# Kernel optimization log

Measured on AMD Instinct MI355X. Metric: run time of the kernel, lower is better.

The kernel has to match this reference:

```python
import jax, jax.numpy as jnp
import numpy as np

N_NODES = 20000
N_EDGES = 150000


def _nnconv(x, src, dst, edge_attr, nn_W, nn_b, root, bias, in_c, out_c):
    # Edge-conditioned conv (PyG NNConv, aggr='add'):
    #   W_e = edge_nn(edge_attr_e).reshape(in_c, out_c)
    #   out_i = sum_{e: dst(e)=i} x_{src(e)} @ W_e + x_i @ root + bias
    E = edge_attr.shape[0]
    W = (edge_attr @ nn_W.T + nn_b).reshape(E, in_c, out_c)  # [E, in_c, out_c]
    xj = x[src]                                              # gather [E, in_c]
    msg = jnp.einsum('ei,eio->eo', xj, W)                    # per-edge matmul
    aggr = jax.ops.segment_sum(msg, dst, num_segments=x.shape[0])
    return aggr + x @ root + bias


def setup_inputs() -> dict:
    key = jax.random.key(0)
    ks = jax.random.split(key, 20)

    def glorot(k, shape):
        fan = sum(shape)
        return jax.random.normal(k, shape, dtype=jnp.float32) * jnp.sqrt(2.0 / fan)

    x = jax.random.normal(ks[0], (N_NODES, 2), dtype=jnp.float32)
    edge_index = jax.random.randint(ks[1], (2, N_EDGES), 0, N_NODES, dtype=jnp.int64)
    edge_attr = jax.random.normal(ks[2], (N_EDGES, 2), dtype=jnp.float32)

    return {
        'x': x, 'edge_index': edge_index, 'edge_attr': edge_attr,
        # conv1: in=2, out=32, edge-net Linear(2, 64)
        'nn1_W': glorot(ks[3], (64, 2)), 'nn1_b': jnp.zeros((64,), jnp.float32),
        'root1': glorot(ks[4], (2, 32)), 'b1': jnp.zeros((32,), jnp.float32),
        # conv2: in=32, out=32, edge-net Linear(2, 1024)
        'nn2_W': glorot(ks[5], (1024, 2)), 'nn2_b': jnp.zeros((1024,), jnp.float32),
        'root2': glorot(ks[6], (32, 32)), 'b2': jnp.zeros((32,), jnp.float32),
        # conv3: in=32, out=32, edge-net Linear(2, 1024)
        'nn3_W': glorot(ks[7], (1024, 2)), 'nn3_b': jnp.zeros((1024,), jnp.float32),
        'root3': glorot(ks[8], (32, 32)), 'b3': jnp.zeros((32,), jnp.float32),
        # dense head
        'fc1_W': glorot(ks[9], (32, 32)), 'fc1_b': jnp.zeros((32,), jnp.float32),
        'fc2_W': glorot(ks[10], (1, 32)), 'fc2_b': jnp.zeros((1,), jnp.float32),
    }


def reference(x, edge_index, edge_attr,
              nn1_W, nn1_b, root1, b1,
              nn2_W, nn2_b, root2, b2,
              nn3_W, nn3_b, root3, b3,
              fc1_W, fc1_b, fc2_W, fc2_b):
    src, dst = edge_index[0], edge_index[1]
    h = jax.nn.relu(_nnconv(x, src, dst, edge_attr, nn1_W, nn1_b, root1, b1, 2, 32))
    h = jax.nn.relu(_nnconv(h, src, dst, edge_attr, nn2_W, nn2_b, root2, b2, 32, 32))
    h = jax.nn.relu(_nnconv(h, src, dst, edge_attr, nn3_W, nn3_b, root3, b3, 32, 32))
    h = jax.nn.relu(h @ fc1_W.T + fc1_b)
    return h @ fc2_W.T + fc2_b  # [N_NODES, 1]
```

## Files before the change

kernel.cpp:

```cpp
#include <hip/hip_runtime.h>


#define CAP 32

typedef float f32x4 __attribute__((ext_vector_type(4)));
typedef short s16x8 __attribute__((ext_vector_type(8)));

__device__ __forceinline__ unsigned short f2bf(float x) {
    unsigned u = __float_as_uint(x);
    unsigned r = u + 0x7FFFu + ((u >> 16) & 1u);
    return (unsigned short)(r >> 16);
}
__device__ __forceinline__ float bf2f(unsigned short h) {
    return __uint_as_float(((unsigned)h) << 16);
}

__global__ __launch_bounds__(256) void zero_kernel(int* p, int n) {
    int i = blockIdx.x * 256 + threadIdx.x;
    if (i < n) p[i] = 0;
}

__global__ __launch_bounds__(256) void scatter_kernel(
    const int* __restrict__ src, const int* __restrict__ dst,
    const float* __restrict__ ea, int* __restrict__ cnt,
    int4* __restrict__ edges, int E) {
    int tid = blockIdx.x * 256 + threadIdx.x;
    int T = gridDim.x * 256;
#pragma unroll 4
    for (int k = 0; k < 4; ++k) {
        int e = tid + k * T;
        if (e < E) {
            int d = dst[e];
            int p = atomicAdd(&cnt[d], 1);
            if (p < CAP) {
                float2 a = ((const float2*)ea)[e];
                int s = src[e];
                int4 ed;
                ed.x = s;
                ed.y = __float_as_int(a.x);
                ed.z = __float_as_int(a.y);
                ed.w = s * 32;
                edges[((size_t)d << 5) + p] = ed;
            }
        }
    }
}

__global__ __launch_bounds__(256) void conv1_kernel(
    const float* __restrict__ x, const int* __restrict__ cnt,
    const int4* __restrict__ edges, const float* __restrict__ nnW,
    const float* __restrict__ nnb, const float* __restrict__ root,
    const float* __restrict__ bias, float* __restrict__ hout, int N) {
    int tid = threadIdx.x;
    int g = tid >> 5, lane = tid & 31;
    int n = blockIdx.x * 8 + g;
    if (n >= N) return;
    int deg = cnt[n];
    deg = (deg < CAP) ? deg : CAP;
    const int4* ep = &edges[(size_t)n << 5];
    float p0 = 0, p1 = 0, q0 = 0, q1 = 0, r0 = 0, r1 = 0;
    for (int p = 0; p < deg; p += 8) {
        int m = deg - p;
        m = (m > 8) ? 8 : m;
        int4 e[8];
        float2 xv[8];
#pragma unroll
        for (int k = 0; k < 8; ++k)
            if (k < m) e[k] = ep[p + k];
#pragma unroll
        for (int k = 0; k < 8; ++k)
            if (k < m) xv[k] = ((const float2*)x)[e[k].x];
#pragma unroll
        for (int k = 0; k < 8; ++k)
            if (k < m) {
                float a0 = __int_as_float(e[k].y), a1 = __int_as_float(e[k].z);
                p0 = fmaf(a0, xv[k].x, p0);
                p1 = fmaf(a0, xv[k].y, p1);
                q0 = fmaf(a1, xv[k].x, q0);
                q1 = fmaf(a1, xv[k].y, q1);
                r0 += xv[k].x;
                r1 += xv[k].y;
            }
    }
    float acc = bias[lane];
    acc = fmaf(p0, nnW[lane * 2], acc);
    acc = fmaf(p1, nnW[(32 + lane) * 2], acc);
    acc = fmaf(q0, nnW[lane * 2 + 1], acc);
    acc = fmaf(q1, nnW[(32 + lane) * 2 + 1], acc);
    acc = fmaf(r0, nnb[lane], acc);
    acc = fmaf(r1, nnb[32 + lane], acc);
    float2 xn = ((const float2*)x)[n];
    acc = fmaf(xn.x, root[lane], acc);
    acc = fmaf(xn.y, root[32 + lane], acc);
    hout[n * 32 + lane] = fmaxf(acc, 0.f);
}

template <int BS>
__device__ __forceinline__ void stage_weights(
    const float* __restrict__ nnW, const float* __restrict__ nnb,
    const float* __restrict__ root, unsigned short (*Whi)[32][32],
    unsigned short (*Wlo)[32][32], int t) {
    for (int idx = t; idx < 4096; idx += BS) {
        int kc = idx >> 10, r = idx & 1023, k = r >> 5, o = r & 31;
        float v = (kc == 0)   ? nnW[(k * 32 + o) * 2]
                  : (kc == 1) ? nnW[(k * 32 + o) * 2 + 1]
                  : (kc == 2) ? nnb[k * 32 + o]
                              : root[k * 32 + o];
        unsigned short hb = f2bf(v);
        Whi[kc][o][k] = hb;
        Wlo[kc][o][k] = f2bf(v - bf2f(hb));
    }
}

#define MFMA_BF16 __builtin_amdgcn_mfma_f32_16x16x32_bf16

__device__ __forceinline__ void gather_to_lds(
    const float* __restrict__ h, const int* __restrict__ cnt,
    const int4* __restrict__ edges, float (*Sl)[132], int base, int t, int N) {
    int g = t >> 5, lane = t & 31;
    int n = base + g;
    float s0 = 0, s1 = 0, s2 = 0, s3 = 0;
    if (n < N) {
        int deg = cnt[n];
        deg = (deg < CAP) ? deg : CAP;
        const int4* ep = &edges[(size_t)n << 5];
        for (int p = 0; p < deg; p += 8) {
            int m = deg - p;
            m = (m > 8) ? 8 : m;
            int4 e[8];
            float hv[8];
#pragma unroll
            for (int k = 0; k < 8; ++k)
                if (k < m) e[k] = ep[p + k];
#pragma unroll
            for (int k = 0; k < 8; ++k)
                if (k < m) hv[k] = h[e[k].w + lane];
#pragma unroll
            for (int k = 0; k < 8; ++k)
                if (k < m) {
                    s0 = fmaf(__int_as_float(e[k].y), hv[k], s0);
                    s1 = fmaf(__int_as_float(e[k].z), hv[k], s1);
                    s2 += hv[k];
                }
        }
        s3 = h[n * 32 + lane];
    }
    Sl[g][lane] = s0;
    Sl[g][32 + lane] = s1;
    Sl[g][64 + lane] = s2;
    Sl[g][96 + lane] = s3;
}

__device__ __forceinline__ void tile_mfma(
    const float (*Sl)[132], const unsigned short (*Whi)[32][32],
    const unsigned short (*Wlo)[32][32], int q, int c, f32x4* acc0, f32x4* acc1) {
#pragma unroll
    for (int kc = 0; kc < 4; ++kc) {
        const float* sp = &Sl[c][kc * 32 + q * 8];
        s16x8 ah, al;
#pragma unroll
        for (int e = 0; e < 8; ++e) {
            float v = sp[e];
            unsigned short hb = f2bf(v);
            ah[e] = (short)hb;
            al[e] = (short)f2bf(v - bf2f(hb));
        }
        s16x8 bh0 = *reinterpret_cast<const s16x8*>(&Whi[kc][c][q * 8]);
        s16x8 bl0 = *reinterpret_cast<const s16x8*>(&Wlo[kc][c][q * 8]);
        s16x8 bh1 = *reinterpret_cast<const s16x8*>(&Whi[kc][16 + c][q * 8]);
        s16x8 bl1 = *reinterpret_cast<const s16x8*>(&Wlo[kc][16 + c][q * 8]);
        *acc0 = MFMA_BF16(ah, bh0, *acc0, 0, 0, 0);
        *acc0 = MFMA_BF16(al, bh0, *acc0, 0, 0, 0);
        *acc0 = MFMA_BF16(ah, bl0, *acc0, 0, 0, 0);
        *acc1 = MFMA_BF16(ah, bh1, *acc1, 0, 0, 0);
        *acc1 = MFMA_BF16(al, bh1, *acc1, 0, 0, 0);
        *acc1 = MFMA_BF16(ah, bl1, *acc1, 0, 0, 0);
    }
}

__global__ __launch_bounds__(512) void fused2_kernel(
    const float* __restrict__ h, const int* __restrict__ cnt,
    const int4* __restrict__ edges, const float* __restrict__ nnW,
    const float* __restrict__ nnb, const float* __restrict__ root,
    const float* __restrict__ bias, float* __restrict__ hout, int N) {
    __shared__ unsigned short Whi[4][32][32], Wlo[4][32][32];
    __shared__ float Sl[16][132];
    int t = threadIdx.x;
    int base = blockIdx.x * 16;
    stage_weights<512>(nnW, nnb, root, Whi, Wlo, t);
    gather_to_lds(h, cnt, edges, Sl, base, t, N);
    __syncthreads();
    if (t < 64) {
        int q = t >> 4, c = t & 15;
        f32x4 acc0 = {0.f, 0.f, 0.f, 0.f}, acc1 = {0.f, 0.f, 0.f, 0.f};
        tile_mfma(Sl, Whi, Wlo, q, c, &acc0, &acc1);
        float bb0 = bias[c], bb1 = bias[16 + c];
#pragma unroll
        for (int rr = 0; rr < 4; ++rr) {
            int n = base + q * 4 + rr;
            if (n < N) {
                hout[(size_t)n * 32 + c] = fmaxf(acc0[rr] + bb0, 0.f);
                hout[(size_t)n * 32 + 16 + c] = fmaxf(acc1[rr] + bb1, 0.f);
            }
        }
    }
}

__global__ __launch_bounds__(512) void fused3_kernel(
    const float* __restrict__ h, const int* __restrict__ cnt,
    const int4* __restrict__ edges, const float* __restrict__ nnW,
    const float* __restrict__ nnb, const float* __restrict__ root,
    const float* __restrict__ bias, const float* __restrict__ fc1W,
    const float* __restrict__ fc1b, const float* __restrict__ fc2W,
    const float* __restrict__ fc2b, float* __restrict__ out, int N) {
    __shared__ unsigned short Whi[4][32][32], Wlo[4][32][32];
    __shared__ float Sl[16][132];
    __shared__ unsigned short Th[16][32], Tl[16][32];
    int t = threadIdx.x;
    int base = blockIdx.x * 16;
    stage_weights<512>(nnW, nnb, root, Whi, Wlo, t);
    gather_to_lds(h, cnt, edges, Sl, base, t, N);
    __syncthreads();
    int q = t >> 4, c = t & 15;
    if (t < 64) {
        f32x4 acc0 = {0.f, 0.f, 0.f, 0.f}, acc1 = {0.f, 0.f, 0.f, 0.f};
        tile_mfma(Sl, Whi, Wlo, q, c, &acc0, &acc1);
        float bb0 = bias[c], bb1 = bias[16 + c];
#pragma unroll
        for (int rr = 0; rr < 4; ++rr) {
            int row = q * 4 + rr;
            float v0 = fmaxf(acc0[rr] + bb0, 0.f);
            float v1 = fmaxf(acc1[rr] + bb1, 0.f);
            unsigned short hb;
            hb = f2bf(v0); Th[row][c] = hb;      Tl[row][c] = f2bf(v0 - bf2f(hb));
            hb = f2bf(v1); Th[row][16 + c] = hb; Tl[row][16 + c] = f2bf(v1 - bf2f(hb));
        }
    }
    __syncthreads();
    if (t < 64) {
        s16x8 fh[2], fl[2];
#pragma unroll
        for (int nc = 0; nc < 2; ++nc)
#pragma unroll
            for (int e = 0; e < 8; ++e) {
                float v = fc1W[(nc * 16 + c) * 32 + q * 8 + e];
                unsigned short hb = f2bf(v);
                fh[nc][e] = (short)hb;
                fl[nc][e] = (short)f2bf(v - bf2f(hb));
            }
        s16x8 hh = *reinterpret_cast<const s16x8*>(&Th[c][q * 8]);
        s16x8 hl = *reinterpret_cast<const s16x8*>(&Tl[c][q * 8]);
        f32x4 z0 = {0.f, 0.f, 0.f, 0.f}, z1 = {0.f, 0.f, 0.f, 0.f};
        z0 = MFMA_BF16(hh, fh[0], z0, 0, 0, 0);
        z0 = MFMA_BF16(hl, fh[0], z0, 0, 0, 0);
        z0 = MFMA_BF16(hh, fl[0], z0, 0, 0, 0);
        z1 = MFMA_BF16(hh, fh[1], z1, 0, 0, 0);
        z1 = MFMA_BF16(hl, fh[1], z1, 0, 0, 0);
        z1 = MFMA_BF16(hh, fl[1], z1, 0, 0, 0);
        float f1b0 = fc1b[c], f1b1 = fc1b[16 + c];
        float w20 = fc2W[c], w21 = fc2W[16 + c];
        float f2b = fc2b[0];
#pragma unroll
        for (int rr = 0; rr < 4; ++rr) {
            float zz0 = fmaxf(z0[rr] + f1b0, 0.f);
            float zz1 = fmaxf(z1[rr] + f1b1, 0.f);
            float v = fmaf(zz0, w20, zz1 * w21);
            v += __shfl_xor(v, 1);
            v += __shfl_xor(v, 2);
            v += __shfl_xor(v, 4);
            v += __shfl_xor(v, 8);
            int n = base + q * 4 + rr;
            if (c == 0 && n < N) out[n] = v + f2b;
        }
    }
}

static inline size_t align256(size_t v) { return (v + 255) & ~(size_t)255; }

extern "C" void kernel_launch(void* const* d_in, const int* in_sizes, int n_in,
                              void* d_out, int out_size, void* d_ws, size_t ws_size,
                              hipStream_t stream) {
    const float* x = (const float*)d_in[0];
    const int* ei = (const int*)d_in[1];
    const float* ea = (const float*)d_in[2];
    const float* nn1W = (const float*)d_in[3];
    const float* nn1b = (const float*)d_in[4];
    const float* root1 = (const float*)d_in[5];
    const float* b1 = (const float*)d_in[6];
    const float* nn2W = (const float*)d_in[7];
    const float* nn2b = (const float*)d_in[8];
    const float* root2 = (const float*)d_in[9];
    const float* b2 = (const float*)d_in[10];
    const float* nn3W = (const float*)d_in[11];
    const float* nn3b = (const float*)d_in[12];
    const float* root3 = (const float*)d_in[13];
    const float* b3 = (const float*)d_in[14];
    const float* fc1W = (const float*)d_in[15];
    const float* fc1b = (const float*)d_in[16];
    const float* fc2W = (const float*)d_in[17];
    const float* fc2b = (const float*)d_in[18];

    const int N = in_sizes[0] / 2;
    const int E = in_sizes[2] / 2;
    const int* src = ei;
    const int* dst = ei + E;

    char* w = (char*)d_ws;
    int* cnt = (int*)w;     w += align256((size_t)N * 4);
    int4* edges = (int4*)w; w += align256((size_t)N * CAP * 16);
    float* h1 = (float*)w;  w += align256((size_t)N * 32 * 4);
    float* h2 = (float*)w;  w += align256((size_t)N * 32 * 4);

    float* out = (float*)d_out;

    zero_kernel<<<(N + 255) / 256, 256, 0, stream>>>(cnt, N);

    int sb = (E + 1023) / 1024;
    scatter_kernel<<<sb, 256, 0, stream>>>(src, dst, ea, cnt, edges, E);

    int gb = (N + 7) / 8;
    int fb = (N + 15) / 16;
    conv1_kernel<<<gb, 256, 0, stream>>>(x, cnt, edges, nn1W, nn1b, root1, b1, h1, N);
    fused2_kernel<<<fb, 512, 0, stream>>>(h1, cnt, edges, nn2W, nn2b, root2, b2, h2, N);
    fused3_kernel<<<fb, 512, 0, stream>>>(h2, cnt, edges, nn3W, nn3b, root3, b3,
                                          fc1W, fc1b, fc2W, fc2b, out, N);
}
```

Measured before the change: 77.31 us.

## Zero-pad edge buckets and load edge records once per lane with shuffles

The zero kernel now clears the whole edge-bucket array along with the counts, so unused slots hold zero weight and offset zero. Each aggregation loop can then run to a multiple of 8 with no per-edge bounds checks. Each lane loads one edge record, broadcasts fields with shuffles, and uses a stored 1.0 weight for the sum term. The cost is zeroing about 10 MB of buckets on every call, plus extra gathers on the padded slots.

```diff
diff --git a/kernel.cpp b/kernel.cpp
--- a/kernel.cpp
+++ b/kernel.cpp
@@ -15,9 +15,11 @@
     return __uint_as_float(((unsigned)h) << 16);
 }
 
-__global__ __launch_bounds__(256) void zero_kernel(int* p, int n) {
+__global__ __launch_bounds__(256) void zero_kernel(int4* p, int n4) {
     int i = blockIdx.x * 256 + threadIdx.x;
-    if (i < n) p[i] = 0;
+    int gt = gridDim.x * 256;
+    int4 z = {0, 0, 0, 0};
+    for (; i < n4; i += gt) p[i] = z;
 }
 
 __global__ __launch_bounds__(256) void scatter_kernel(
@@ -34,12 +36,11 @@
             int p = atomicAdd(&cnt[d], 1);
             if (p < CAP) {
                 float2 a = ((const float2*)ea)[e];
-                int s = src[e];
                 int4 ed;
-                ed.x = s;
+                ed.x = __float_as_int(1.0f);
                 ed.y = __float_as_int(a.x);
                 ed.z = __float_as_int(a.y);
-                ed.w = s * 32;
+                ed.w = src[e] * 32;
                 edges[((size_t)d << 5) + p] = ed;
             }
         }
@@ -57,30 +58,30 @@
     if (n >= N) return;
     int deg = cnt[n];
     deg = (deg < CAP) ? deg : CAP;
+    int deg8 = (deg + 7) & ~7;
     const int4* ep = &edges[(size_t)n << 5];
+    int4 rec = ep[lane];
     float p0 = 0, p1 = 0, q0 = 0, q1 = 0, r0 = 0, r1 = 0;
-    for (int p = 0; p < deg; p += 8) {
-        int m = deg - p;
-        m = (m > 8) ? 8 : m;
-        int4 e[8];
+    for (int p = 0; p < deg8; p += 8) {
         float2 xv[8];
-#pragma unroll
-        for (int k = 0; k < 8; ++k)
-            if (k < m) e[k] = ep[p + k];
-#pragma unroll
-        for (int k = 0; k < 8; ++k)
-            if (k < m) xv[k] = ((const float2*)x)[e[k].x];
-#pragma unroll
-        for (int k = 0; k < 8; ++k)
-            if (k < m) {
-                float a0 = __int_as_float(e[k].y), a1 = __int_as_float(e[k].z);
-                p0 = fmaf(a0, xv[k].x, p0);
-                p1 = fmaf(a0, xv[k].y, p1);
-                q0 = fmaf(a1, xv[k].x, q0);
-                q1 = fmaf(a1, xv[k].y, q1);
-                r0 += xv[k].x;
-                r1 += xv[k].y;
-            }
+        float a0[8], a1[8], ww[8];
+#pragma unroll
+        for (int j = 0; j < 8; ++j) {
+            int off = __shfl(rec.w, p + j, 32);
+            a0[j] = __int_as_float(__shfl(rec.y, p + j, 32));
+            a1[j] = __int_as_float(__shfl(rec.z, p + j, 32));
+            ww[j] = __int_as_float(__shfl(rec.x, p + j, 32));
+            xv[j] = ((const float2*)x)[off >> 5];
+        }
+#pragma unroll
+        for (int j = 0; j < 8; ++j) {
+            p0 = fmaf(a0[j], xv[j].x, p0);
+            p1 = fmaf(a0[j], xv[j].y, p1);
+            q0 = fmaf(a1[j], xv[j].x, q0);
+            q1 = fmaf(a1[j], xv[j].y, q1);
+            r0 = fmaf(ww[j], xv[j].x, r0);
+            r1 = fmaf(ww[j], xv[j].y, r1);
+        }
     }
     float acc = bias[lane];
     acc = fmaf(p0, nnW[lane * 2], acc);
@@ -123,27 +124,27 @@
     if (n < N) {
         int deg = cnt[n];
         deg = (deg < CAP) ? deg : CAP;
+        int deg8 = (deg + 7) & ~7;
         const int4* ep = &edges[(size_t)n << 5];
-        for (int p = 0; p < deg; p += 8) {
-            int m = deg - p;
-            m = (m > 8) ? 8 : m;
-            int4 e[8];
-            float hv[8];
-#pragma unroll
-            for (int k = 0; k < 8; ++k)
-                if (k < m) e[k] = ep[p + k];
-#pragma unroll
-            for (int k = 0; k < 8; ++k)
-                if (k < m) hv[k] = h[e[k].w + lane];
-#pragma unroll
-            for (int k = 0; k < 8; ++k)
-                if (k < m) {
-                    s0 = fmaf(__int_as_float(e[k].y), hv[k], s0);
-                    s1 = fmaf(__int_as_float(e[k].z), hv[k], s1);
-                    s2 += hv[k];
-                }
-        }
+        int4 rec = ep[lane];
         s3 = h[n * 32 + lane];
+        for (int p = 0; p < deg8; p += 8) {
+            float hv[8], a0[8], a1[8], ww[8];
+#pragma unroll
+            for (int j = 0; j < 8; ++j) {
+                int off = __shfl(rec.w, p + j, 32);
+                a0[j] = __int_as_float(__shfl(rec.y, p + j, 32));
+                a1[j] = __int_as_float(__shfl(rec.z, p + j, 32));
+                ww[j] = __int_as_float(__shfl(rec.x, p + j, 32));
+                hv[j] = h[off + lane];
+            }
+#pragma unroll
+            for (int j = 0; j < 8; ++j) {
+                s0 = fmaf(a0[j], hv[j], s0);
+                s1 = fmaf(a1[j], hv[j], s1);
+                s2 = fmaf(ww[j], hv[j], s2);
+            }
+        }
     }
     Sl[g][lane] = s0;
     Sl[g][32 + lane] = s1;
@@ -308,12 +309,14 @@
     char* w = (char*)d_ws;
     int* cnt = (int*)w;     w += align256((size_t)N * 4);
     int4* edges = (int4*)w; w += align256((size_t)N * CAP * 16);
+    char* zero_end = w;
     float* h1 = (float*)w;  w += align256((size_t)N * 32 * 4);
     float* h2 = (float*)w;  w += align256((size_t)N * 32 * 4);
 
     float* out = (float*)d_out;
 
-    zero_kernel<<<(N + 255) / 256, 256, 0, stream>>>(cnt, N);
+    int n4 = (int)((zero_end - (char*)cnt) / 16);
+    zero_kernel<<<512, 256, 0, stream>>>((int4*)cnt, n4);
 
     int sb = (E + 1023) / 1024;
     scatter_kernel<<<sb, 256, 0, stream>>>(src, dst, ea, cnt, edges, E);
```

After: 70.58 us. 1.1x faster.
